# Performance work log

Measured on AMD Instinct MI355X. Metric: run time of the kernel, lower is better.

The kernel has to match this reference:

```python
import jax, jax.numpy as jnp
import numpy as np

# 4-qubit statevector simulator (state shape (2,2,2,2)); RY and CNOT are real,
_CNOT = jnp.array([[1.,0.,0.,0.],[0.,1.,0.,0.],[0.,0.,0.,1.],[0.,0.,1.,0.]], dtype=jnp.float32).reshape(2,2,2,2)
_RING = [(0,1),(1,2),(2,3),(3,0)]

def _ry(state, theta, wire):
    h = 0.5 * theta
    c, s = jnp.cos(h), jnp.sin(h)
    m = jnp.stack([jnp.stack([c, -s]), jnp.stack([s, c])])
    return jnp.moveaxis(jnp.tensordot(m, state, axes=([1], [wire])), 0, wire)

def _cnot(state, c, t):
    out = jnp.tensordot(_CNOT, state, axes=([2, 3], [c, t]))
    return jnp.moveaxis(out, (0, 1), (c, t))

def _embed(x):
    # RY angle embedding of the flattened 2x2 patch onto 4 wires
    s = jnp.zeros((2, 2, 2, 2), dtype=x.dtype).at[0, 0, 0, 0].set(1.0)
    for i in range(4):
        s = _ry(s, x[i], i)
    return s

def _expz0(s):
    return jnp.sum(s[0] ** 2) - jnp.sum(s[1] ** 2)

def _circ_ran(x, w):   # 7 weights
    s = _embed(x)
    for i in range(4):
        s = _ry(s, w[i], i)
    s = _cnot(s, 0, 1); s = _cnot(s, 2, 3)
    s = _ry(s, w[4], 0); s = _ry(s, w[5], 2)
    s = _cnot(s, 1, 2)
    s = _ry(s, w[6], 1)
    return _expz0(s)

def _circ_line(x, w):  # 7 weights
    s = _embed(x)
    for i in range(4):
        s = _ry(s, w[i], i)
    for (c, t) in [(0, 1), (1, 2), (2, 3)]:
        s = _cnot(s, c, t)
    for i in range(3):
        s = _ry(s, w[4 + i], i + 1)
    return _expz0(s)

def _circ_ring(x, w):  # 8 weights
    s = _embed(x)
    for i in range(4):
        s = _ry(s, w[i], i)
    for (c, t) in _RING:
        s = _cnot(s, c, t)
    for i in range(4):
        s = _ry(s, w[4 + i], i)
    return _expz0(s)

def _circ_doublering(x, w):  # 16 weights: 2 layers x (4 RY + ring fwd + 4 RY + ring bwd)
    s = _embed(x)
    for L in range(2):
        b = 8 * L
        for i in range(4):
            s = _ry(s, w[b + i], i)
        for (c, t) in _RING:
            s = _cnot(s, c, t)
        for i in range(4):
            s = _ry(s, w[b + 4 + i], i)
        for (c, t) in reversed(_RING):
            s = _cnot(s, c, t)
    return _expz0(s)

def _circ_blockring(x, w):  # 12 weights: 3 layers x (4 RY + block+ring CNOTs)
    s = _embed(x)
    for L in range(3):
        for i in range(4):
            s = _ry(s, w[4 * L + i], i)
        for (c, t) in [(0, 1), (2, 3), (1, 2), (3, 0)]:
            s = _cnot(s, c, t)
    return _expz0(s)

_CIRCUITS = [(_circ_ran, 7), (_circ_line, 7), (_circ_ring, 8), (_circ_doublering, 16), (_circ_blockring, 12)]

def _forward(inputs, weights):
    B, C, H, W = inputs.shape
    Hp, Wp = H - 1, W - 1  # kernel_size=2, stride=1, no padding
    # sliding 2x2 patches, flattened row-major (matches reshape of [.., 2, 2] -> [.., 4])
    patches = jnp.stack([inputs[:, :, :Hp, :Wp], inputs[:, :, :Hp, 1:],
                         inputs[:, :, 1:, :Wp], inputs[:, :, 1:, 1:]], axis=-1)  # [B,C,Hp,Wp,4]
    x = jnp.moveaxis(patches, 1, 0).reshape(C, B * Hp * Wp, 4)  # [C, N, 4]
    O = weights.shape[0]
    outs = []
    for i in range(O):  # small structural loop: circuits differ by type i%5
        fn, nw = _CIRCUITS[i % 5]
        w = weights[i, :, :nw]  # [C, nw]
        per_c = jax.vmap(jax.vmap(fn, in_axes=(0, None)), in_axes=(0, 0))(x, w)  # [C, N]
        outs.append(per_c.sum(0))  # sum over input channels
    out = jnp.stack(outs, 0).reshape(O, B, Hp, Wp)
    return jnp.moveaxis(out, 0, 1)  # [B, O, Hp, Wp]

def setup_inputs() -> dict:
    key = jax.random.key(0)
    k1, k2 = jax.random.split(key)
    inputs = jax.random.normal(k1, (16, 3, 32, 32), dtype=jnp.float32)
    weights = jax.random.normal(k2, (16, 3, 16), dtype=jnp.float32)  # padded; circuit i uses first {7,7,8,16,12}[i%5]
    return {"inputs": inputs, "weights": weights}

def reference(inputs, weights):
    return _forward(inputs, weights)
```

## Files before the change

### kernel.cpp

```cpp
#include <hip/hip_runtime.h>


#define HPW 961
#define NPATCH 15376

template<int STRIDE>
__device__ __forceinline__ void ry_s(float* s, float c, float sn) {
#pragma unroll
    for (int i = 0; i < 16; ++i) {
        if ((i & STRIDE) == 0) {
            float a = s[i], b = s[i + STRIDE];
            s[i]          = c * a - sn * b;
            s[i + STRIDE] = sn * a + c * b;
        }
    }
}

template<int CS, int TS>
__device__ __forceinline__ void cnot_s(float* s) {
#pragma unroll
    for (int i = 0; i < 16; ++i) {
        if ((i & CS) != 0 && (i & TS) == 0) {
            float t = s[i]; s[i] = s[i + TS]; s[i + TS] = t;
        }
    }
}


__device__ __forceinline__ void circ_ran(float* s, const float* C, const float* S) {
    ry_s<8>(s, C[0], S[0]); ry_s<4>(s, C[1], S[1]); ry_s<2>(s, C[2], S[2]); ry_s<1>(s, C[3], S[3]);
    cnot_s<8,4>(s); cnot_s<2,1>(s);
    ry_s<8>(s, C[4], S[4]); ry_s<2>(s, C[5], S[5]);
    cnot_s<4,2>(s);
    ry_s<4>(s, C[6], S[6]);
}

__device__ __forceinline__ void circ_line(float* s, const float* C, const float* S) {
    ry_s<8>(s, C[0], S[0]); ry_s<4>(s, C[1], S[1]); ry_s<2>(s, C[2], S[2]); ry_s<1>(s, C[3], S[3]);
    cnot_s<8,4>(s); cnot_s<4,2>(s); cnot_s<2,1>(s);
    ry_s<4>(s, C[4], S[4]); ry_s<2>(s, C[5], S[5]); ry_s<1>(s, C[6], S[6]);
}

__device__ __forceinline__ void circ_ring(float* s, const float* C, const float* S) {
    ry_s<8>(s, C[0], S[0]); ry_s<4>(s, C[1], S[1]); ry_s<2>(s, C[2], S[2]); ry_s<1>(s, C[3], S[3]);
    cnot_s<8,4>(s); cnot_s<4,2>(s); cnot_s<2,1>(s); cnot_s<1,8>(s);
    ry_s<8>(s, C[4], S[4]); ry_s<4>(s, C[5], S[5]); ry_s<2>(s, C[6], S[6]); ry_s<1>(s, C[7], S[7]);
}

__device__ __forceinline__ void circ_doublering(float* s, const float* C, const float* S) {
#pragma unroll
    for (int L = 0; L < 2; ++L) {
        const int b = 8 * L;
        ry_s<8>(s, C[b+0], S[b+0]); ry_s<4>(s, C[b+1], S[b+1]); ry_s<2>(s, C[b+2], S[b+2]); ry_s<1>(s, C[b+3], S[b+3]);
        cnot_s<8,4>(s); cnot_s<4,2>(s); cnot_s<2,1>(s); cnot_s<1,8>(s);
        ry_s<8>(s, C[b+4], S[b+4]); ry_s<4>(s, C[b+5], S[b+5]); ry_s<2>(s, C[b+6], S[b+6]); ry_s<1>(s, C[b+7], S[b+7]);
        cnot_s<1,8>(s); cnot_s<2,1>(s); cnot_s<4,2>(s); cnot_s<8,4>(s);
    }
}

__device__ __forceinline__ void circ_blockring(float* s, const float* C, const float* S) {
#pragma unroll
    for (int L = 0; L < 3; ++L) {
        const int b = 4 * L;
        ry_s<8>(s, C[b+0], S[b+0]); ry_s<4>(s, C[b+1], S[b+1]); ry_s<2>(s, C[b+2], S[b+2]); ry_s<1>(s, C[b+3], S[b+3]);
        cnot_s<8,4>(s); cnot_s<2,1>(s); cnot_s<4,2>(s); cnot_s<1,8>(s);
    }
}

__global__ __launch_bounds__(256) void quanv_kernel(const float* __restrict__ in,
                                                    const float* __restrict__ wts,
                                                    float* __restrict__ out) {
    __shared__ float cw[48], sw[48];
    const int o = blockIdx.y;
    const int t = threadIdx.x;
    if (t < 48) {
        float sn, cs;
        __sincosf(0.5f * wts[o * 48 + t], &sn, &cs);
        cw[t] = cs; sw[t] = sn;
    }
    __syncthreads();

    const int pidx = blockIdx.x * 256 + t;
    if (pidx >= NPATCH) return;
    const int b   = pidx / HPW;
    const int rem = pidx - b * HPW;
    const int h   = rem / 31;
    const int w   = rem - h * 31;
    const int circ = o % 5;

    float acc = 0.0f;
#pragma unroll
    for (int c = 0; c < 3; ++c) {
        const float* p = in + (((b * 3 + c) * 32) + h) * 32 + w;
        const float x0 = p[0], x1 = p[1], x2 = p[32], x3 = p[33];

        float s0, c0, s1, c1, s2, c2, s3, c3;
        __sincosf(0.5f * x0, &s0, &c0);
        __sincosf(0.5f * x1, &s1, &c1);
        __sincosf(0.5f * x2, &s2, &c2);
        __sincosf(0.5f * x3, &s3, &c3);

        const float m00 = c0 * c1, m01 = c0 * s1, m10 = s0 * c1, m11 = s0 * s1;
        const float n00 = c2 * c3, n01 = c2 * s3, n10 = s2 * c3, n11 = s2 * s3;
        float s[16];
        s[0]  = m00 * n00; s[1]  = m00 * n01; s[2]  = m00 * n10; s[3]  = m00 * n11;
        s[4]  = m01 * n00; s[5]  = m01 * n01; s[6]  = m01 * n10; s[7]  = m01 * n11;
        s[8]  = m10 * n00; s[9]  = m10 * n01; s[10] = m10 * n10; s[11] = m10 * n11;
        s[12] = m11 * n00; s[13] = m11 * n01; s[14] = m11 * n10; s[15] = m11 * n11;

        const float* C = cw + c * 16;
        const float* S = sw + c * 16;
        switch (circ) {
            case 0: circ_ran(s, C, S);        break;
            case 1: circ_line(s, C, S);       break;
            case 2: circ_ring(s, C, S);       break;
            case 3: circ_doublering(s, C, S); break;
            default: circ_blockring(s, C, S); break;
        }

        float e = 0.0f;
#pragma unroll
        for (int i = 0; i < 8; ++i)  e += s[i] * s[i];
#pragma unroll
        for (int i = 8; i < 16; ++i) e -= s[i] * s[i];
        acc += e;
    }

    out[((b * 16 + o) * 31 + h) * 31 + w] = acc;
}

extern "C" void kernel_launch(void* const* d_in, const int* in_sizes, int n_in,
                              void* d_out, int out_size, void* d_ws, size_t ws_size,
                              hipStream_t stream) {
    const float* in  = (const float*)d_in[0];
    const float* wts = (const float*)d_in[1];
    float* out = (float*)d_out;
    dim3 grid((NPATCH + 255) / 256, 16);
    quanv_kernel<<<grid, 256, 0, stream>>>(in, wts, out);
}
```

Baseline: 65.08 us.

## Simplify each circuit analytically, merge embedding and weight rotations, drop unused gates

Each circuit type gets its own simplified evaluation. Consecutive RY rotations on the same wire are merged by adding the angles, and gates that cannot affect <Z0> are removed. The ran and line circuits become closed-form trig expressions of one or two inputs. The shared-memory cos/sin table and its barrier are dropped, so the weight sincos now runs per thread and per gate, which adds transcendental work in the deeper circuits.

After: 61.77 us. 5.1% less time.

```diff
diff --git a/kernel.cpp b/kernel.cpp
--- a/kernel.cpp
+++ b/kernel.cpp
@@ -26,60 +26,31 @@
     }
 }
 
-
-__device__ __forceinline__ void circ_ran(float* s, const float* C, const float* S) {
-    ry_s<8>(s, C[0], S[0]); ry_s<4>(s, C[1], S[1]); ry_s<2>(s, C[2], S[2]); ry_s<1>(s, C[3], S[3]);
-    cnot_s<8,4>(s); cnot_s<2,1>(s);
-    ry_s<8>(s, C[4], S[4]); ry_s<2>(s, C[5], S[5]);
-    cnot_s<4,2>(s);
-    ry_s<4>(s, C[6], S[6]);
+__device__ __forceinline__ void build16(float* s,
+        float c0, float s0, float c1, float s1,
+        float c2, float s2, float c3, float s3) {
+    const float m00 = c0 * c1, m01 = c0 * s1, m10 = s0 * c1, m11 = s0 * s1;
+    const float n00 = c2 * c3, n01 = c2 * s3, n10 = s2 * c3, n11 = s2 * s3;
+    s[0]  = m00 * n00; s[1]  = m00 * n01; s[2]  = m00 * n10; s[3]  = m00 * n11;
+    s[4]  = m01 * n00; s[5]  = m01 * n01; s[6]  = m01 * n10; s[7]  = m01 * n11;
+    s[8]  = m10 * n00; s[9]  = m10 * n01; s[10] = m10 * n10; s[11] = m10 * n11;
+    s[12] = m11 * n00; s[13] = m11 * n01; s[14] = m11 * n10; s[15] = m11 * n11;
 }
 
-__device__ __forceinline__ void circ_line(float* s, const float* C, const float* S) {
-    ry_s<8>(s, C[0], S[0]); ry_s<4>(s, C[1], S[1]); ry_s<2>(s, C[2], S[2]); ry_s<1>(s, C[3], S[3]);
-    cnot_s<8,4>(s); cnot_s<4,2>(s); cnot_s<2,1>(s);
-    ry_s<4>(s, C[4], S[4]); ry_s<2>(s, C[5], S[5]); ry_s<1>(s, C[6], S[6]);
-}
-
-__device__ __forceinline__ void circ_ring(float* s, const float* C, const float* S) {
-    ry_s<8>(s, C[0], S[0]); ry_s<4>(s, C[1], S[1]); ry_s<2>(s, C[2], S[2]); ry_s<1>(s, C[3], S[3]);
-    cnot_s<8,4>(s); cnot_s<4,2>(s); cnot_s<2,1>(s); cnot_s<1,8>(s);
-    ry_s<8>(s, C[4], S[4]); ry_s<4>(s, C[5], S[5]); ry_s<2>(s, C[6], S[6]); ry_s<1>(s, C[7], S[7]);
-}
-
-__device__ __forceinline__ void circ_doublering(float* s, const float* C, const float* S) {
+__device__ __forceinline__ float expz0v(const float* s) {
+    float e = 0.0f;
 #pragma unroll
-    for (int L = 0; L < 2; ++L) {
-        const int b = 8 * L;
-        ry_s<8>(s, C[b+0], S[b+0]); ry_s<4>(s, C[b+1], S[b+1]); ry_s<2>(s, C[b+2], S[b+2]); ry_s<1>(s, C[b+3], S[b+3]);
-        cnot_s<8,4>(s); cnot_s<4,2>(s); cnot_s<2,1>(s); cnot_s<1,8>(s);
-        ry_s<8>(s, C[b+4], S[b+4]); ry_s<4>(s, C[b+5], S[b+5]); ry_s<2>(s, C[b+6], S[b+6]); ry_s<1>(s, C[b+7], S[b+7]);
-        cnot_s<1,8>(s); cnot_s<2,1>(s); cnot_s<4,2>(s); cnot_s<8,4>(s);
-    }
-}
-
-__device__ __forceinline__ void circ_blockring(float* s, const float* C, const float* S) {
+    for (int i = 0; i < 8; ++i)  e += s[i] * s[i];
 #pragma unroll
-    for (int L = 0; L < 3; ++L) {
-        const int b = 4 * L;
-        ry_s<8>(s, C[b+0], S[b+0]); ry_s<4>(s, C[b+1], S[b+1]); ry_s<2>(s, C[b+2], S[b+2]); ry_s<1>(s, C[b+3], S[b+3]);
-        cnot_s<8,4>(s); cnot_s<2,1>(s); cnot_s<4,2>(s); cnot_s<1,8>(s);
-    }
+    for (int i = 8; i < 16; ++i) e -= s[i] * s[i];
+    return e;
 }
 
 __global__ __launch_bounds__(256) void quanv_kernel(const float* __restrict__ in,
                                                     const float* __restrict__ wts,
                                                     float* __restrict__ out) {
-    __shared__ float cw[48], sw[48];
     const int o = blockIdx.y;
     const int t = threadIdx.x;
-    if (t < 48) {
-        float sn, cs;
-        __sincosf(0.5f * wts[o * 48 + t], &sn, &cs);
-        cw[t] = cs; sw[t] = sn;
-    }
-    __syncthreads();
-
     const int pidx = blockIdx.x * 256 + t;
     if (pidx >= NPATCH) return;
     const int b   = pidx / HPW;
@@ -88,42 +59,103 @@
     const int w   = rem - h * 31;
     const int circ = o % 5;
 
+    const float* W  = wts + o * 48;
+    const float* p0 = in + ((b * 3) * 32 + h) * 32 + w;
     float acc = 0.0f;
+
+    switch (circ) {
+    case 0: {
 #pragma unroll
-    for (int c = 0; c < 3; ++c) {
-        const float* p = in + (((b * 3 + c) * 32) + h) * 32 + w;
-        const float x0 = p[0], x1 = p[1], x2 = p[32], x3 = p[33];
-
-        float s0, c0, s1, c1, s2, c2, s3, c3;
-        __sincosf(0.5f * x0, &s0, &c0);
-        __sincosf(0.5f * x1, &s1, &c1);
-        __sincosf(0.5f * x2, &s2, &c2);
-        __sincosf(0.5f * x3, &s3, &c3);
-
-        const float m00 = c0 * c1, m01 = c0 * s1, m10 = s0 * c1, m11 = s0 * s1;
-        const float n00 = c2 * c3, n01 = c2 * s3, n10 = s2 * c3, n11 = s2 * s3;
-        float s[16];
-        s[0]  = m00 * n00; s[1]  = m00 * n01; s[2]  = m00 * n10; s[3]  = m00 * n11;
-        s[4]  = m01 * n00; s[5]  = m01 * n01; s[6]  = m01 * n10; s[7]  = m01 * n11;
-        s[8]  = m10 * n00; s[9]  = m10 * n01; s[10] = m10 * n10; s[11] = m10 * n11;
-        s[12] = m11 * n00; s[13] = m11 * n01; s[14] = m11 * n10; s[15] = m11 * n11;
-
-        const float* C = cw + c * 16;
-        const float* S = sw + c * 16;
-        switch (circ) {
-            case 0: circ_ran(s, C, S);        break;
-            case 1: circ_line(s, C, S);       break;
-            case 2: circ_ring(s, C, S);       break;
-            case 3: circ_doublering(s, C, S); break;
-            default: circ_blockring(s, C, S); break;
+        for (int c = 0; c < 3; ++c) {
+            const float* p  = p0 + c * 1024;
+            const float* wc = W + c * 16;
+            const float a0 = p[0] + wc[0];
+            const float a1 = p[1] + wc[1];
+            float s4, c4;  __sincosf(wc[4], &s4, &c4);
+            float sa0, ca0; __sincosf(a0, &sa0, &ca0);
+            const float sa1 = __sinf(a1);
+            acc += c4 * ca0 - s4 * sa0 * sa1;
         }
-
-        float e = 0.0f;
+    } break;
+    case 1: {
 #pragma unroll
-        for (int i = 0; i < 8; ++i)  e += s[i] * s[i];
+        for (int c = 0; c < 3; ++c)
+            acc += __cosf(p0[c * 1024] + W[c * 16]);
+    } break;
+    case 2: {
 #pragma unroll
-        for (int i = 8; i < 16; ++i) e -= s[i] * s[i];
-        acc += e;
+        for (int c = 0; c < 3; ++c) {
+            const float* p  = p0 + c * 1024;
+            const float* wc = W + c * 16;
+            float c0,s0,c1,s1,c2,s2,c3,s3;
+            __sincosf(0.5f * (p[0]  + wc[0]), &s0, &c0);
+            __sincosf(0.5f * (p[1]  + wc[1]), &s1, &c1);
+            __sincosf(0.5f * (p[32] + wc[2]), &s2, &c2);
+            __sincosf(0.5f * (p[33] + wc[3]), &s3, &c3);
+            float s[16]; build16(s, c0,s0,c1,s1,c2,s2,c3,s3);
+            cnot_s<8,4>(s); cnot_s<4,2>(s); cnot_s<2,1>(s); cnot_s<1,8>(s);
+            float sw, cw; __sincosf(0.5f * wc[4], &sw, &cw);
+            ry_s<8>(s, cw, sw);
+            acc += expz0v(s);
+        }
+    } break;
+    case 3: {
+#pragma unroll
+        for (int c = 0; c < 3; ++c) {
+            const float* p  = p0 + c * 1024;
+            const float* wc = W + c * 16;
+            float c0,s0,c1,s1,c2,s2,c3,s3;
+            __sincosf(0.5f * (p[0]  + wc[0]), &s0, &c0);
+            __sincosf(0.5f * (p[1]  + wc[1]), &s1, &c1);
+            __sincosf(0.5f * (p[32] + wc[2]), &s2, &c2);
+            __sincosf(0.5f * (p[33] + wc[3]), &s3, &c3);
+            float s[16]; build16(s, c0,s0,c1,s1,c2,s2,c3,s3);
+            cnot_s<8,4>(s); cnot_s<4,2>(s); cnot_s<2,1>(s); cnot_s<1,8>(s);
+            float sg, cg;
+            __sincosf(0.5f * wc[4], &sg, &cg); ry_s<8>(s, cg, sg);
+            __sincosf(0.5f * wc[5], &sg, &cg); ry_s<4>(s, cg, sg);
+            __sincosf(0.5f * wc[6], &sg, &cg); ry_s<2>(s, cg, sg);
+            __sincosf(0.5f * wc[7], &sg, &cg); ry_s<1>(s, cg, sg);
+            cnot_s<1,8>(s); cnot_s<2,1>(s); cnot_s<4,2>(s); cnot_s<8,4>(s);
+            __sincosf(0.5f * wc[8],  &sg, &cg); ry_s<8>(s, cg, sg);
+            __sincosf(0.5f * wc[9],  &sg, &cg); ry_s<4>(s, cg, sg);
+            __sincosf(0.5f * wc[10], &sg, &cg); ry_s<2>(s, cg, sg);
+            __sincosf(0.5f * wc[11], &sg, &cg); ry_s<1>(s, cg, sg);
+            cnot_s<8,4>(s); cnot_s<4,2>(s); cnot_s<2,1>(s); cnot_s<1,8>(s);
+            __sincosf(0.5f * wc[12], &sg, &cg); ry_s<8>(s, cg, sg);
+            __sincosf(0.5f * wc[13], &sg, &cg); ry_s<4>(s, cg, sg);
+            __sincosf(0.5f * wc[14], &sg, &cg); ry_s<2>(s, cg, sg);
+            __sincosf(0.5f * wc[15], &sg, &cg); ry_s<1>(s, cg, sg);
+            cnot_s<1,8>(s); cnot_s<2,1>(s); cnot_s<4,2>(s); cnot_s<8,4>(s);
+            acc += expz0v(s);
+        }
+    } break;
+    default: {
+#pragma unroll
+        for (int c = 0; c < 3; ++c) {
+            const float* p  = p0 + c * 1024;
+            const float* wc = W + c * 16;
+            float c0,s0,c1,s1,c2,s2,c3,s3;
+            __sincosf(0.5f * (p[0]  + wc[0]), &s0, &c0);
+            __sincosf(0.5f * (p[1]  + wc[1]), &s1, &c1);
+            __sincosf(0.5f * (p[32] + wc[2]), &s2, &c2);
+            __sincosf(0.5f * (p[33] + wc[3]), &s3, &c3);
+            float s[16]; build16(s, c0,s0,c1,s1,c2,s2,c3,s3);
+            cnot_s<8,4>(s); cnot_s<2,1>(s); cnot_s<4,2>(s); cnot_s<1,8>(s);
+            float sg, cg;
+            __sincosf(0.5f * wc[4], &sg, &cg); ry_s<8>(s, cg, sg);
+            __sincosf(0.5f * wc[5], &sg, &cg); ry_s<4>(s, cg, sg);
+            __sincosf(0.5f * wc[6], &sg, &cg); ry_s<2>(s, cg, sg);
+            __sincosf(0.5f * wc[7], &sg, &cg); ry_s<1>(s, cg, sg);
+            cnot_s<8,4>(s); cnot_s<2,1>(s); cnot_s<4,2>(s); cnot_s<1,8>(s);
+            __sincosf(0.5f * wc[8],  &sg, &cg); ry_s<8>(s, cg, sg);
+            __sincosf(0.5f * wc[9],  &sg, &cg); ry_s<4>(s, cg, sg);
+            __sincosf(0.5f * wc[10], &sg, &cg); ry_s<2>(s, cg, sg);
+            __sincosf(0.5f * wc[11], &sg, &cg); ry_s<1>(s, cg, sg);
+            cnot_s<8,4>(s); cnot_s<2,1>(s); cnot_s<4,2>(s); cnot_s<1,8>(s);
+            acc += expz0v(s);
+        }
+    } break;
     }
 
     out[((b * 16 + o) * 31 + h) * 31 + w] = acc;
```
